# Performance work log

Hardware: AMD Instinct MI355X
Metric: run time of the kernel (lower is better)

The kernel has to match this reference:

```python
import jax, jax.numpy as jnp
import numpy as np

B, T, H, W, C = 2, 8, 64, 64, 256
HEADS = 8
WS = 8


def setup_inputs() -> dict:
    key = jax.random.key(0)
    k1, k2, k3 = jax.random.split(key, 3)
    x = jax.random.normal(k1, (B, T, H, W, C), dtype=jnp.float32)
    qkv_w = jax.random.normal(k2, (C, 3 * C), dtype=jnp.float32) * (C ** -0.5)
    proj_w = jax.random.normal(k3, (C, C), dtype=jnp.float32) * (C ** -0.5)
    proj_b = jnp.zeros((C,), dtype=jnp.float32)
    return {"x": x, "qkv_w": qkv_w, "proj_w": proj_w, "proj_b": proj_b}


def reference(x, qkv_w, proj_w, proj_b):
    b, t, h, w, c = x.shape
    hn, wn = h // WS, w // WS
    dh = c // HEADS
    scale = dh ** -0.5
    # window partition: (B,T,H,W,C) -> (B*hn*wn, T*WS*WS, C)
    xw = x.reshape(b, t, hn, WS, wn, WS, c)
    xw = jnp.transpose(xw, (0, 2, 4, 1, 3, 5, 6)).reshape(-1, t * WS * WS, c)
    bw, n, _ = xw.shape
    qkv = (xw @ qkv_w).reshape(bw, n, 3, HEADS, dh)
    qkv = jnp.transpose(qkv, (2, 0, 3, 1, 4))  # (3, Bw, heads, N, dh)
    q, k, v = qkv[0], qkv[1], qkv[2]
    attn = jax.nn.softmax(jnp.einsum("bhnd,bhmd->bhnm", q, k) * scale, axis=-1)
    out = jnp.einsum("bhnm,bhmd->bhnd", attn, v)
    out = jnp.transpose(out, (0, 2, 1, 3)).reshape(bw, n, c)
    out = out @ proj_w + proj_b
    # window reverse
    out = out.reshape(b, hn, wn, t, WS, WS, c)
    out = jnp.transpose(out, (0, 3, 1, 4, 2, 5, 6)).reshape(b, t, h, w, c)
    return out
```

## Files before the change

### kernel.cpp

```cpp
#include <hip/hip_runtime.h>


typedef __bf16 bf16x8 __attribute__((ext_vector_type(8)));
typedef float f32x4 __attribute__((ext_vector_type(4)));
typedef float f32x16 __attribute__((ext_vector_type(16)));

#define NTOK 512
#define DH 32
#define CDIM 256
#define C3 768

__device__ __forceinline__ unsigned short f2b(float f) {
  unsigned u = __builtin_bit_cast(unsigned, f);
  unsigned r = u + 0x7fffu + ((u >> 16) & 1u);
  return (unsigned short)(r >> 16);
}

__device__ __forceinline__ unsigned pk2(float a, float b) {
  __bf16 x = (__bf16)a, y = (__bf16)b;
  return (unsigned)__builtin_bit_cast(unsigned short, x) |
         ((unsigned)__builtin_bit_cast(unsigned short, y) << 16);
}

__global__ void k_prep(const float* __restrict__ qkv_w, const float* __restrict__ proj_w,
                       unsigned short* __restrict__ wqT, unsigned short* __restrict__ wpT) {
  const float QS = 0.2550540254f;
  int idx = blockIdx.x * 256 + threadIdx.x;
  int stride = gridDim.x * 256;
  for (int i = idx; i < C3 * CDIM; i += stride) {
    int n = i >> 8, kk = i & 255;
    float f = qkv_w[kk * C3 + n];
    if (n < 256) f *= QS;
    wqT[i] = f2b(f);
  }
  for (int i = idx; i < CDIM * CDIM; i += stride) {
    int n = i >> 8, kk = i & 255;
    wpT[i] = f2b(proj_w[kk * CDIM + n]);
  }
}

__global__ __launch_bounds__(256, 2) void k_qkv(
    const float* __restrict__ x, const unsigned short* __restrict__ wqT,
    unsigned short* __restrict__ qo, unsigned short* __restrict__ ko,
    unsigned short* __restrict__ vo) {
  extern __shared__ char smem[];
  unsigned short (*As)[264] = (unsigned short (*)[264])smem;
  int tid = threadIdx.x;
  int mtile = blockIdx.x;
  int bw = mtile >> 2;
  int n0 = (mtile & 3) << 7;
  int bb = bw >> 6, hi = (bw >> 3) & 7, wi = bw & 7;

  {
    int row = tid >> 1;
    int n = n0 + row;
    int tt = n >> 6, ii = (n >> 3) & 7, jj = n & 7;
    const float* src = x + ((((long)(bb * 8 + tt)) * 64 + (hi * 8 + ii)) * 64 + (wi * 8 + jj)) * 256;
    int fb = (tid & 1) * 4;
#pragma unroll
    for (int u = 0; u < 32; ++u) {
      int f = fb + u * 8;
      float4 d = *(const float4*)(src + f);
      __bf16 h0 = (__bf16)d.x, h1 = (__bf16)d.y, h2 = (__bf16)d.z, h3 = (__bf16)d.w;
      __bf16* dst = (__bf16*)&As[row][f];
      dst[0] = h0; dst[1] = h1; dst[2] = h2; dst[3] = h3;
    }
  }
  __syncthreads();

  int wid = tid >> 6, lane = tid & 63;
  int lg = lane >> 4, lr = lane & 15;
  int wr = wid >> 1, wc = wid & 1;
  unsigned short* Ts = (unsigned short*)(smem + 67584) + wid * 16 * 88;

  for (int nt = 0; nt < 6; ++nt) {
    f32x4 acc[4][4];
#pragma unroll
    for (int a = 0; a < 4; ++a)
#pragma unroll
      for (int b2 = 0; b2 < 4; ++b2) acc[a][b2] = (f32x4){0.f, 0.f, 0.f, 0.f};

    const unsigned short* bb2 = wqT + ((long)(nt * 128 + wc * 64)) * 256;
    for (int kk = 0; kk < 256; kk += 32) {
      bf16x8 af[4], bfr[4];
#pragma unroll
      for (int ni = 0; ni < 4; ++ni)
        bfr[ni] = *(const bf16x8*)(bb2 + (ni * 16 + lr) * 256 + kk + lg * 8);
#pragma unroll
      for (int mi = 0; mi < 4; ++mi)
        af[mi] = *(const bf16x8*)&As[wr * 64 + mi * 16 + lr][kk + lg * 8];
#pragma unroll
      for (int mi = 0; mi < 4; ++mi)
#pragma unroll
        for (int ni = 0; ni < 4; ++ni)
          acc[mi][ni] = __builtin_amdgcn_mfma_f32_16x16x32_bf16(af[mi], bfr[ni], acc[mi][ni], 0, 0, 0);
    }

    if (nt < 4) {
      unsigned short* dst = (nt < 2) ? qo : ko;
      int head0 = (nt * 4 + wc * 2) & 7;
      long base0 = ((long)(bw * 8 + head0)) * 16384;
      long base1 = ((long)(bw * 8 + head0 + 1)) * 16384;
      int row = lane >> 2, c2 = lane & 3;
#pragma unroll
      for (int mi = 0; mi < 4; ++mi) {
#pragma unroll
        for (int ni = 0; ni < 4; ++ni)
#pragma unroll
          for (int r = 0; r < 4; ++r) {
            __bf16 hv = (__bf16)acc[mi][ni][r];
            Ts[(lg * 4 + r) * 88 + ni * 16 + lr] = __builtin_bit_cast(unsigned short, hv);
          }
        int n = n0 + wr * 64 + mi * 16 + row;
        long toff = ((long)((n >> 5) * 4 + c2)) * 256 + (n & 31) * 8;
        uint4 d0 = *(const uint4*)&Ts[row * 88 + c2 * 8];
        *(uint4*)&dst[base0 + toff] = d0;
        uint4 d1 = *(const uint4*)&Ts[row * 88 + 32 + c2 * 8];
        *(uint4*)&dst[base1 + toff] = d1;
      }
    } else {
#pragma unroll
      for (int ni = 0; ni < 4; ++ni) {
        int c = nt * 128 + wc * 64 + ni * 16 + lr;
        int d = c & 31;
        long base = ((long)(bw * 8 + ((c >> 5) & 7))) * 16384;
#pragma unroll
        for (int mi = 0; mi < 4; ++mi) {
          int m = n0 + wr * 64 + mi * 16 + lg * 4;
          long off = base + ((long)((m >> 5) * 4 + ((m >> 4) & 1) * 2 + ((m >> 3) & 1)) * 32 + d) * 8 + (m & 7);
          ushort4 w;
          __bf16 v0 = (__bf16)acc[mi][ni][0], v1 = (__bf16)acc[mi][ni][1];
          __bf16 v2 = (__bf16)acc[mi][ni][2], v3 = (__bf16)acc[mi][ni][3];
          w.x = __builtin_bit_cast(unsigned short, v0);
          w.y = __builtin_bit_cast(unsigned short, v1);
          w.z = __builtin_bit_cast(unsigned short, v2);
          w.w = __builtin_bit_cast(unsigned short, v3);
          *(ushort4*)&vo[off] = w;
        }
      }
    }
  }
}

__global__ __launch_bounds__(256, 2) void k_attn(
    const unsigned short* __restrict__ qs0, const unsigned short* __restrict__ ks0,
    const unsigned short* __restrict__ vs0, unsigned short* __restrict__ og) {
  extern __shared__ char smem[];
  int bh = blockIdx.x, tid = threadIdx.x;
  const unsigned short* kg = ks0 + (long)bh * 16384;
  const unsigned short* vg = vs0 + (long)bh * 16384;
#pragma unroll
  for (int i = 0; i < 8; ++i) {
    int ci = tid + i * 256;
    *(uint4*)(smem + ci * 16) = *(const uint4*)(kg + ci * 8);
    *(uint4*)(smem + 32768 + ci * 16) = *(const uint4*)(vg + ci * 8);
  }
  __syncthreads();

  int wid = tid >> 6, lane = tid & 63;
  int l31 = lane & 31, h = lane >> 5;
  const unsigned short* qb = qs0 + (long)bh * 16384;
  unsigned short* ob = og + (long)bh * 16384;
  const f32x16 z16 = {0.f,0.f,0.f,0.f,0.f,0.f,0.f,0.f,0.f,0.f,0.f,0.f,0.f,0.f,0.f,0.f};

  bf16x8 qf[4][2];
#pragma unroll
  for (int qt = 0; qt < 4; ++qt)
#pragma unroll
    for (int ks = 0; ks < 2; ++ks)
      qf[qt][ks] = *(const bf16x8*)(qb + ((wid * 4 + qt) * 4 + ks * 2 + h) * 256 + l31 * 8);

  f32x16 o[4];
  float ps[4];
#pragma unroll
  for (int qt = 0; qt < 4; ++qt) { o[qt] = z16; ps[qt] = 0.f; }

  for (int mt = 0; mt < 16; ++mt) {
    bf16x8 k0 = *(const bf16x8*)(smem + (mt * 4 + h) * 512 + l31 * 16);
    bf16x8 k1 = *(const bf16x8*)(smem + (mt * 4 + 2 + h) * 512 + l31 * 16);
    bf16x8 v0 = *(const bf16x8*)(smem + 32768 + (mt * 4 + h) * 512 + l31 * 16);
    bf16x8 v1 = *(const bf16x8*)(smem + 32768 + (mt * 4 + 2 + h) * 512 + l31 * 16);
#pragma unroll
    for (int qt = 0; qt < 4; ++qt) {
      f32x16 s = __builtin_amdgcn_mfma_f32_32x32x16_bf16(k0, qf[qt][0], z16, 0, 0, 0);
      s = __builtin_amdgcn_mfma_f32_32x32x16_bf16(k1, qf[qt][1], s, 0, 0, 0);
      float p[16];
#pragma unroll
      for (int r = 0; r < 16; ++r) p[r] = __builtin_amdgcn_exp2f(s[r]);
      ps[qt] += ((((p[0] + p[1]) + (p[2] + p[3])) + ((p[4] + p[5]) + (p[6] + p[7]))) +
                 (((p[8] + p[9]) + (p[10] + p[11])) + ((p[12] + p[13]) + (p[14] + p[15]))));
      unsigned w0 = pk2(p[0], p[1]),  w1 = pk2(p[2], p[3]);
      unsigned w2 = pk2(p[4], p[5]),  w3 = pk2(p[6], p[7]);
      unsigned w4 = pk2(p[8], p[9]),  w5 = pk2(p[10], p[11]);
      unsigned w6 = pk2(p[12], p[13]), w7 = pk2(p[14], p[15]);
      asm("v_permlane32_swap_b32 %0, %1" : "+v"(w0), "+v"(w2));
      asm("v_permlane32_swap_b32 %0, %1" : "+v"(w1), "+v"(w3));
      asm("v_permlane32_swap_b32 %0, %1" : "+v"(w4), "+v"(w6));
      asm("v_permlane32_swap_b32 %0, %1" : "+v"(w5), "+v"(w7));
      uint4 pb0u; pb0u.x = w0; pb0u.y = w1; pb0u.z = w2; pb0u.w = w3;
      uint4 pb1u; pb1u.x = w4; pb1u.y = w5; pb1u.z = w6; pb1u.w = w7;
      bf16x8 pb0 = __builtin_bit_cast(bf16x8, pb0u);
      bf16x8 pb1 = __builtin_bit_cast(bf16x8, pb1u);
      o[qt] = __builtin_amdgcn_mfma_f32_32x32x16_bf16(v0, pb0, o[qt], 0, 0, 0);
      o[qt] = __builtin_amdgcn_mfma_f32_32x32x16_bf16(v1, pb1, o[qt], 0, 0, 0);
    }
  }

#pragma unroll
  for (int qt = 0; qt < 4; ++qt) {
    float sum = ps[qt] + __shfl_xor(ps[qt], 32, 64);
    float rcp = 1.0f / sum;
    int q = (wid * 4 + qt) * 32 + l31;
#pragma unroll
    for (int s4 = 0; s4 < 4; ++s4) {
      __bf16 b0 = (__bf16)(o[qt][s4 * 4 + 0] * rcp);
      __bf16 b1 = (__bf16)(o[qt][s4 * 4 + 1] * rcp);
      __bf16 b2 = (__bf16)(o[qt][s4 * 4 + 2] * rcp);
      __bf16 b3 = (__bf16)(o[qt][s4 * 4 + 3] * rcp);
      ushort4 w;
      w.x = __builtin_bit_cast(unsigned short, b0);
      w.y = __builtin_bit_cast(unsigned short, b1);
      w.z = __builtin_bit_cast(unsigned short, b2);
      w.w = __builtin_bit_cast(unsigned short, b3);
      *(ushort4*)(ob + q * 32 + s4 * 8 + h * 4) = w;
    }
  }
}

__global__ __launch_bounds__(256, 2) void k_proj(
    const unsigned short* __restrict__ og, const unsigned short* __restrict__ wpT,
    const float* __restrict__ pb, float* __restrict__ out) {
  extern __shared__ char smem[];
  unsigned short (*As)[264] = (unsigned short (*)[264])smem;
  int tid = threadIdx.x;
  int mtile = blockIdx.x;
  int bw = mtile >> 2;
  int n0 = (mtile & 3) << 7;
  int bb = bw >> 6, hi = (bw >> 3) & 7, wi = bw & 7;

  {
    int row = tid >> 1, hf = tid & 1;
#pragma unroll
    for (int h4 = 0; h4 < 4; ++h4) {
      int h = hf * 4 + h4;
      const uint4* asrc = (const uint4*)(og + (((long)(bw * 8 + h)) * NTOK + n0 + row) * DH);
      uint4 d0 = asrc[0], d1 = asrc[1], d2 = asrc[2], d3 = asrc[3];
      *(uint4*)&As[row][h * 32]      = d0;
      *(uint4*)&As[row][h * 32 + 8]  = d1;
      *(uint4*)&As[row][h * 32 + 16] = d2;
      *(uint4*)&As[row][h * 32 + 24] = d3;
    }
  }
  __syncthreads();

  int wid = tid >> 6, lane = tid & 63;
  int lg = lane >> 4, lr = lane & 15;
  int wr = wid >> 1, wc = wid & 1;

  for (int nt = 0; nt < 2; ++nt) {
    f32x4 acc[4][4];
#pragma unroll
    for (int a = 0; a < 4; ++a)
#pragma unroll
      for (int b2 = 0; b2 < 4; ++b2) acc[a][b2] = (f32x4){0.f, 0.f, 0.f, 0.f};

    const unsigned short* bb2 = wpT + ((long)(nt * 128 + wc * 64)) * 256;
    for (int kk = 0; kk < 256; kk += 32) {
      bf16x8 af[4], bfr[4];
#pragma unroll
      for (int ni = 0; ni < 4; ++ni)
        bfr[ni] = *(const bf16x8*)(bb2 + (ni * 16 + lr) * 256 + kk + lg * 8);
#pragma unroll
      for (int mi = 0; mi < 4; ++mi)
        af[mi] = *(const bf16x8*)&As[wr * 64 + mi * 16 + lr][kk + lg * 8];
#pragma unroll
      for (int mi = 0; mi < 4; ++mi)
#pragma unroll
        for (int ni = 0; ni < 4; ++ni)
          acc[mi][ni] = __builtin_amdgcn_mfma_f32_16x16x32_bf16(af[mi], bfr[ni], acc[mi][ni], 0, 0, 0);
    }
#pragma unroll
    for (int ni = 0; ni < 4; ++ni) {
      int c = nt * 128 + wc * 64 + ni * 16 + lr;
      float bias = pb[c];
#pragma unroll
      for (int mi = 0; mi < 4; ++mi) {
        int nbase = n0 + wr * 64 + mi * 16 + lg * 4;
#pragma unroll
        for (int r = 0; r < 4; ++r) {
          int n = nbase + r;
          int tt = n >> 6, ii = (n >> 3) & 7, jj = n & 7;
          long off = ((((long)(bb * 8 + tt)) * 64 + (hi * 8 + ii)) * 64 + (wi * 8 + jj)) * 256 + c;
          out[off] = acc[mi][ni][r] + bias;
        }
      }
    }
  }
}

extern "C" void kernel_launch(void* const* d_in, const int* in_sizes, int n_in,
                              void* d_out, int out_size, void* d_ws, size_t ws_size,
                              hipStream_t stream) {
  const float* x      = (const float*)d_in[0];
  const float* qkv_w  = (const float*)d_in[1];
  const float* proj_w = (const float*)d_in[2];
  const float* proj_b = (const float*)d_in[3];
  float* out = (float*)d_out;
  char* ws = (char*)d_ws;

  unsigned short* wqT = (unsigned short*)(ws);
  unsigned short* wpT = (unsigned short*)(ws + 393216);
  unsigned short* Q   = (unsigned short*)(ws + 524288);
  unsigned short* K   = (unsigned short*)(ws + 524288 + 1L * 33554432);
  unsigned short* V   = (unsigned short*)(ws + 524288 + 2L * 33554432);
  unsigned short* O   = (unsigned short*)(ws + 524288 + 3L * 33554432);

  (void)hipFuncSetAttribute((const void*)k_qkv,  hipFuncAttributeMaxDynamicSharedMemorySize, 78848);
  (void)hipFuncSetAttribute((const void*)k_attn, hipFuncAttributeMaxDynamicSharedMemorySize, 65536);
  (void)hipFuncSetAttribute((const void*)k_proj, hipFuncAttributeMaxDynamicSharedMemorySize, 67584);

  k_prep<<<256, 256, 0, stream>>>(qkv_w, proj_w, wqT, wpT);
  k_qkv<<<512, 256, 78848, stream>>>(x, wqT, Q, K, V);
  k_attn<<<1024, 256, 65536, stream>>>(Q, K, V, O);
  k_proj<<<512, 256, 67584, stream>>>(O, wpT, proj_b, out);
}
```

Measured before the change: 156.2 us.

## Retile QKV GEMM to 64-row blocks and stage proj weights in LDS

The QKV projection kernel now uses 64-token tiles with 1024 blocks. Each wave covers a 64-column slice across all tokens, iterating three column groups, which cuts LDS use and allows launch bounds of 3 blocks per CU. The output projection kernel now loads each 128x32 weight slice cooperatively into LDS per k-step instead of having every wave read weights directly from global memory. That adds two barriers per k-step in exchange for fewer redundant global weight loads.

```diff
diff --git a/kernel.cpp b/kernel.cpp
--- a/kernel.cpp
+++ b/kernel.cpp
@@ -39,7 +39,7 @@
   }
 }
 
-__global__ __launch_bounds__(256, 2) void k_qkv(
+__global__ __launch_bounds__(256, 3) void k_qkv(
     const float* __restrict__ x, const unsigned short* __restrict__ wqT,
     unsigned short* __restrict__ qo, unsigned short* __restrict__ ko,
     unsigned short* __restrict__ vo) {
@@ -47,19 +47,19 @@
   unsigned short (*As)[264] = (unsigned short (*)[264])smem;
   int tid = threadIdx.x;
   int mtile = blockIdx.x;
-  int bw = mtile >> 2;
-  int n0 = (mtile & 3) << 7;
+  int bw = mtile >> 3;
+  int n0 = (mtile & 7) << 6;
   int bb = bw >> 6, hi = (bw >> 3) & 7, wi = bw & 7;
 
   {
-    int row = tid >> 1;
+    int row = tid >> 2;
     int n = n0 + row;
     int tt = n >> 6, ii = (n >> 3) & 7, jj = n & 7;
     const float* src = x + ((((long)(bb * 8 + tt)) * 64 + (hi * 8 + ii)) * 64 + (wi * 8 + jj)) * 256;
-    int fb = (tid & 1) * 4;
-#pragma unroll
-    for (int u = 0; u < 32; ++u) {
-      int f = fb + u * 8;
+    int fb = (tid & 3) * 4;
+#pragma unroll
+    for (int u = 0; u < 16; ++u) {
+      int f = fb + u * 16;
       float4 d = *(const float4*)(src + f);
       __bf16 h0 = (__bf16)d.x, h1 = (__bf16)d.y, h2 = (__bf16)d.z, h3 = (__bf16)d.w;
       __bf16* dst = (__bf16*)&As[row][f];
@@ -70,17 +70,17 @@
 
   int wid = tid >> 6, lane = tid & 63;
   int lg = lane >> 4, lr = lane & 15;
-  int wr = wid >> 1, wc = wid & 1;
-  unsigned short* Ts = (unsigned short*)(smem + 67584) + wid * 16 * 88;
-
-  for (int nt = 0; nt < 6; ++nt) {
+  unsigned short* Ts = (unsigned short*)(smem + 33792) + wid * 16 * 88;
+
+  for (int it = 0; it < 3; ++it) {
+    int c0 = (it * 4 + wid) * 64;
     f32x4 acc[4][4];
 #pragma unroll
     for (int a = 0; a < 4; ++a)
 #pragma unroll
       for (int b2 = 0; b2 < 4; ++b2) acc[a][b2] = (f32x4){0.f, 0.f, 0.f, 0.f};
 
-    const unsigned short* bb2 = wqT + ((long)(nt * 128 + wc * 64)) * 256;
+    const unsigned short* bb2 = wqT + (long)c0 * 256;
     for (int kk = 0; kk < 256; kk += 32) {
       bf16x8 af[4], bfr[4];
 #pragma unroll
@@ -88,7 +88,7 @@
         bfr[ni] = *(const bf16x8*)(bb2 + (ni * 16 + lr) * 256 + kk + lg * 8);
 #pragma unroll
       for (int mi = 0; mi < 4; ++mi)
-        af[mi] = *(const bf16x8*)&As[wr * 64 + mi * 16 + lr][kk + lg * 8];
+        af[mi] = *(const bf16x8*)&As[mi * 16 + lr][kk + lg * 8];
 #pragma unroll
       for (int mi = 0; mi < 4; ++mi)
 #pragma unroll
@@ -96,12 +96,13 @@
           acc[mi][ni] = __builtin_amdgcn_mfma_f32_16x16x32_bf16(af[mi], bfr[ni], acc[mi][ni], 0, 0, 0);
     }
 
-    if (nt < 4) {
-      unsigned short* dst = (nt < 2) ? qo : ko;
-      int head0 = (nt * 4 + wc * 2) & 7;
+    int which = c0 >> 8;
+    if (which < 2) {
+      unsigned short* dst = (which == 0) ? qo : ko;
+      int head0 = (c0 >> 5) & 7;
       long base0 = ((long)(bw * 8 + head0)) * 16384;
       long base1 = ((long)(bw * 8 + head0 + 1)) * 16384;
-      int row = lane >> 2, c2 = lane & 3;
+      int trow = lane >> 2, c2 = lane & 3;
 #pragma unroll
       for (int mi = 0; mi < 4; ++mi) {
 #pragma unroll
@@ -111,22 +112,22 @@
             __bf16 hv = (__bf16)acc[mi][ni][r];
             Ts[(lg * 4 + r) * 88 + ni * 16 + lr] = __builtin_bit_cast(unsigned short, hv);
           }
-        int n = n0 + wr * 64 + mi * 16 + row;
+        int n = n0 + mi * 16 + trow;
         long toff = ((long)((n >> 5) * 4 + c2)) * 256 + (n & 31) * 8;
-        uint4 d0 = *(const uint4*)&Ts[row * 88 + c2 * 8];
+        uint4 d0 = *(const uint4*)&Ts[trow * 88 + c2 * 8];
         *(uint4*)&dst[base0 + toff] = d0;
-        uint4 d1 = *(const uint4*)&Ts[row * 88 + 32 + c2 * 8];
+        uint4 d1 = *(const uint4*)&Ts[trow * 88 + 32 + c2 * 8];
         *(uint4*)&dst[base1 + toff] = d1;
       }
     } else {
 #pragma unroll
       for (int ni = 0; ni < 4; ++ni) {
-        int c = nt * 128 + wc * 64 + ni * 16 + lr;
+        int c = c0 + ni * 16 + lr;
         int d = c & 31;
         long base = ((long)(bw * 8 + ((c >> 5) & 7))) * 16384;
 #pragma unroll
         for (int mi = 0; mi < 4; ++mi) {
-          int m = n0 + wr * 64 + mi * 16 + lg * 4;
+          int m = n0 + mi * 16 + lg * 4;
           long off = base + ((long)((m >> 5) * 4 + ((m >> 4) & 1) * 2 + ((m >> 3) & 1)) * 32 + d) * 8 + (m & 7);
           ushort4 w;
           __bf16 v0 = (__bf16)acc[mi][ni][0], v1 = (__bf16)acc[mi][ni][1];
@@ -232,6 +233,7 @@
     const float* __restrict__ pb, float* __restrict__ out) {
   extern __shared__ char smem[];
   unsigned short (*As)[264] = (unsigned short (*)[264])smem;
+  unsigned short (*Bs)[40]  = (unsigned short (*)[40])(smem + 128 * 264 * 2);
   int tid = threadIdx.x;
   int mtile = blockIdx.x;
   int bw = mtile >> 2;
@@ -264,15 +266,23 @@
 #pragma unroll
       for (int b2 = 0; b2 < 4; ++b2) acc[a][b2] = (f32x4){0.f, 0.f, 0.f, 0.f};
 
-    const unsigned short* bb2 = wpT + ((long)(nt * 128 + wc * 64)) * 256;
     for (int kk = 0; kk < 256; kk += 32) {
+      __syncthreads();
+      {
+        int brow = tid >> 1, bh2 = tid & 1;
+        const uint4* bs = (const uint4*)(wpT + ((long)(nt * 128 + brow)) * 256 + kk + bh2 * 16);
+        uint4 b0 = bs[0], b1 = bs[1];
+        *(uint4*)&Bs[brow][bh2 * 16] = b0;
+        *(uint4*)&Bs[brow][bh2 * 16 + 8] = b1;
+      }
+      __syncthreads();
       bf16x8 af[4], bfr[4];
-#pragma unroll
-      for (int ni = 0; ni < 4; ++ni)
-        bfr[ni] = *(const bf16x8*)(bb2 + (ni * 16 + lr) * 256 + kk + lg * 8);
 #pragma unroll
       for (int mi = 0; mi < 4; ++mi)
         af[mi] = *(const bf16x8*)&As[wr * 64 + mi * 16 + lr][kk + lg * 8];
+#pragma unroll
+      for (int ni = 0; ni < 4; ++ni)
+        bfr[ni] = *(const bf16x8*)&Bs[wc * 64 + ni * 16 + lr][lg * 8];
 #pragma unroll
       for (int mi = 0; mi < 4; ++mi)
 #pragma unroll
@@ -315,12 +325,12 @@
   unsigned short* V   = (unsigned short*)(ws + 524288 + 2L * 33554432);
   unsigned short* O   = (unsigned short*)(ws + 524288 + 3L * 33554432);
 
-  (void)hipFuncSetAttribute((const void*)k_qkv,  hipFuncAttributeMaxDynamicSharedMemorySize, 78848);
+  (void)hipFuncSetAttribute((const void*)k_qkv,  hipFuncAttributeMaxDynamicSharedMemorySize, 45056);
   (void)hipFuncSetAttribute((const void*)k_attn, hipFuncAttributeMaxDynamicSharedMemorySize, 65536);
-  (void)hipFuncSetAttribute((const void*)k_proj, hipFuncAttributeMaxDynamicSharedMemorySize, 67584);
+  (void)hipFuncSetAttribute((const void*)k_proj, hipFuncAttributeMaxDynamicSharedMemorySize, 77824);
 
   k_prep<<<256, 256, 0, stream>>>(qkv_w, proj_w, wqT, wpT);
-  k_qkv<<<512, 256, 78848, stream>>>(x, wqT, Q, K, V);
+  k_qkv<<<1024, 256, 45056, stream>>>(x, wqT, Q, K, V);
   k_attn<<<1024, 256, 65536, stream>>>(Q, K, V, O);
-  k_proj<<<512, 256, 67584, stream>>>(O, wpT, proj_b, out);
-}
+  k_proj<<<512, 256, 77824, stream>>>(O, wpT, proj_b, out);
+}
```

Result: faster. 151.1 us (-3.3%).
